# Optimization experiments

Hardware: AMD Instinct MI355X
Metric: run time of the kernel (lower is better)

The kernel has to match this reference:

```python
import jax, jax.numpy as jnp
import numpy as np

N_HEAD = 16
LORA_DIM = 16
LORA_ALPHA = 32


def setup_inputs() -> dict:
    key = jax.random.key(0)
    ks = jax.random.split(key, 8)
    B, S, D = 2, 2048, 1024
    std = 0.02
    return {
        "x": jax.random.normal(ks[0], (B, S, D), jnp.float32),
        "c_attn_w": jax.random.normal(ks[1], (D, 3 * D), jnp.float32) * std,
        "c_attn_b": jnp.zeros((3 * D,), jnp.float32),
        "c_proj_w": jax.random.normal(ks[2], (D, D), jnp.float32) * std,
        "c_proj_b": jnp.zeros((D,), jnp.float32),
        "q_a1": jax.random.normal(ks[3], (D, LORA_DIM), jnp.float32) * std,
        "q_a2": jax.random.normal(ks[4], (LORA_DIM, D), jnp.float32) * std,
        "v_a1": jax.random.normal(ks[5], (D, LORA_DIM), jnp.float32) * std,
        "v_a2": jax.random.normal(ks[6], (LORA_DIM, D), jnp.float32) * std,
    }


def reference(x, c_attn_w, c_attn_b, c_proj_w, c_proj_b, q_a1, q_a2, v_a1, v_a2):
    B, S, D = x.shape
    H = N_HEAD
    hd = D // H
    # NOTE: original code uses adapter_dim / adapter_alpha as the scale
    lora_scale = jnp.float32(LORA_DIM / LORA_ALPHA)

    qkv = x @ c_attn_w + c_attn_b                      # [B,S,3D]
    q, k, v = jnp.split(qkv, 3, axis=-1)
    q = q + ((x @ q_a1) @ q_a2) * lora_scale
    v = v + ((x @ v_a1) @ v_a2) * lora_scale

    def heads(t):
        return t.reshape(B, S, H, hd).transpose(0, 2, 1, 3)  # [B,H,S,hd]

    qh, kh, vh = heads(q), heads(k), heads(v)

    w = jnp.einsum('bhqd,bhkd->bhqk', qh, kh) / jnp.sqrt(jnp.float32(hd))
    bias = jnp.tril(jnp.ones((S, S), dtype=w.dtype))   # causal mask
    w = w * bias - jnp.float32(1e10) * (1 - bias)
    w = jax.nn.softmax(w, axis=-1)
    a = jnp.einsum('bhqk,bhkd->bhqd', w, vh)
    a = a.transpose(0, 2, 1, 3).reshape(B, S, D)       # merge heads
    a = a @ c_proj_w + c_proj_b

    present = jnp.stack((kh, vh))                      # [2,B,H,S,hd]
    return a, present
```

## Files before the change

### kernel.cpp

```cpp
#include <hip/hip_runtime.h>

#define T_TOK 4096
#define D_DIM 1024
#define N3    3072
#define S_LEN 2048
#define NH    16
#define HD    64
#define KAUG  1056

#define OUT_A_ELEMS   4194304
#define OUT_KV_ELEMS  4194304

typedef __attribute__((ext_vector_type(8))) short bf16x8;
typedef __attribute__((ext_vector_type(4))) float f32x4;
typedef __attribute__((ext_vector_type(16))) float f32x16;
typedef _Float16 f16x8 __attribute__((ext_vector_type(8)));
typedef _Float16 f16x4 __attribute__((ext_vector_type(4)));

union U4h { unsigned u[4]; f16x8 v; };

#define GHASH(r) ((((r) >> 1) ^ ((r) >> 3)) & 3)

__device__ __forceinline__ unsigned short f2bf(float f) {
    unsigned u = __float_as_uint(f);
    u += 0x7FFFu + ((u >> 16) & 1u);
    return (unsigned short)(u >> 16);
}
__device__ __forceinline__ float bf2f(unsigned short h) {
    return __uint_as_float(((unsigned)h) << 16);
}
__device__ __forceinline__ unsigned cvtpkh(float a, float b) {
    unsigned r;
    asm("v_cvt_pkrtz_f16_f32 %0, %1, %2" : "=v"(r) : "v"(a), "v"(b));
    return r;
}

#define GLL16(gp, lp) __builtin_amdgcn_global_load_lds( \
    (const __attribute__((address_space(1))) unsigned int*)(gp), \
    (__attribute__((address_space(3))) unsigned int*)(lp), 16, 0, 0)

#define MFMA16F(A, B, C) __builtin_amdgcn_mfma_f32_16x16x32_f16(A, B, C, 0, 0, 0)
#define MFMA32F(A, B, C) __builtin_amdgcn_mfma_f32_32x32x16_f16(A, B, C, 0, 0, 0)

__global__ __launch_bounds__(256) void lora1_v2(const float* __restrict__ x,
    const float* __restrict__ qa1, const float* __restrict__ va1,
    float* __restrict__ tq, float* __restrict__ tv) {
    int tid = threadIdx.x;
    int w = tid >> 6;
    int lane = tid & 63;
    int t = blockIdx.x * 4 + w;
    int cg = lane & 7;
    int ks = lane >> 3;
    const float* a1 = (cg < 4) ? qa1 : va1;
    int c4 = (cg & 3) * 4;
    const float* xr = x + (size_t)t * D_DIM + ks * 128;
    const float* ar = a1 + (size_t)(ks * 128) * 16 + c4;
    float4 acc = make_float4(0.f, 0.f, 0.f, 0.f);
#pragma unroll 8
    for (int j = 0; j < 128; ++j) {
        float xv = xr[j];
        float4 av = *(const float4*)&ar[j * 16];
        acc.x = fmaf(xv, av.x, acc.x);
        acc.y = fmaf(xv, av.y, acc.y);
        acc.z = fmaf(xv, av.z, acc.z);
        acc.w = fmaf(xv, av.w, acc.w);
    }
#pragma unroll
    for (int m = 8; m < 64; m <<= 1) {
        acc.x += __shfl_xor(acc.x, m);
        acc.y += __shfl_xor(acc.y, m);
        acc.z += __shfl_xor(acc.z, m);
        acc.w += __shfl_xor(acc.w, m);
    }
    if (lane < 8) {
        float* dst = (cg < 4) ? &tq[t * 16 + c4] : &tv[t * 16 + (cg - 4) * 4];
        *(float4*)dst = acc;
    }
}

__global__ __launch_bounds__(256) void splitA_f16(const float* __restrict__ x,
    const float* __restrict__ tq, const float* __restrict__ tv,
    _Float16* __restrict__ af) {
    int idx = blockIdx.x * 256 + threadIdx.x;
    const int total = T_TOK * (KAUG / 4);
    if (idx >= total) return;
    int t = idx / (KAUG / 4);
    int c4 = (idx - t * (KAUG / 4)) * 4;
    float4 v;
    if (c4 < D_DIM)           v = *(const float4*)&x[(size_t)t * D_DIM + c4];
    else if (c4 < D_DIM + 16) v = *(const float4*)&tq[t * 16 + (c4 - D_DIM)];
    else                      v = *(const float4*)&tv[t * 16 + (c4 - D_DIM - 16)];
    f16x4 h;
    h[0] = (_Float16)v.x; h[1] = (_Float16)v.y;
    h[2] = (_Float16)v.z; h[3] = (_Float16)v.w;
    *(f16x4*)&af[(size_t)t * KAUG + c4] = h;
}

__global__ __launch_bounds__(256) void splitW_f16(const float* __restrict__ w,
    const float* __restrict__ qa2, const float* __restrict__ va2,
    _Float16* __restrict__ bf) {
    __shared__ float T[32][65];
    int bn = blockIdx.x;
    int bk = blockIdx.y;
    int tid = threadIdx.x;
#pragma unroll
    for (int u = 0; u < 2; ++u) {
        int id = tid + 256 * u;
        int kr = id >> 4;
        int n4 = (id & 15) * 4;
        int k = bk * 32 + kr;
        int n = bn * 64 + n4;
        float4 v = make_float4(0.f, 0.f, 0.f, 0.f);
        if (k < D_DIM) {
            v = *(const float4*)&w[(size_t)k * N3 + n];
        } else if (k < D_DIM + 16) {
            if (n < D_DIM) {
                float4 q4 = *(const float4*)&qa2[(k - D_DIM) * D_DIM + n];
                v = make_float4(q4.x * 0.5f, q4.y * 0.5f, q4.z * 0.5f, q4.w * 0.5f);
            }
        } else {
            if (n >= 2 * D_DIM) {
                float4 q4 = *(const float4*)&va2[(k - D_DIM - 16) * D_DIM + (n - 2 * D_DIM)];
                v = make_float4(q4.x * 0.5f, q4.y * 0.5f, q4.z * 0.5f, q4.w * 0.5f);
            }
        }
        T[kr][n4 + 0] = v.x; T[kr][n4 + 1] = v.y;
        T[kr][n4 + 2] = v.z; T[kr][n4 + 3] = v.w;
    }
    __syncthreads();
    int n = tid >> 2;
    int k8 = (tid & 3) * 8;
    f16x8 hv;
#pragma unroll
    for (int j = 0; j < 8; ++j) hv[j] = (_Float16)T[k8 + j][n];
    int nr = bn * 64 + n;
    int gsw = (tid & 3) ^ GHASH(nr);
    size_t ro = (size_t)nr * KAUG + bk * 32 + gsw * 8;
    *(f16x8*)&bf[ro] = hv;
}

__global__ __launch_bounds__(256) void wprep_f16(const float* __restrict__ w,
    _Float16* __restrict__ bf) {
    __shared__ float T[32][65];
    int bn = blockIdx.x;
    int bk = blockIdx.y;
    int tid = threadIdx.x;
#pragma unroll
    for (int u = 0; u < 2; ++u) {
        int id = tid + 256 * u;
        int kr = id >> 4;
        int n4 = (id & 15) * 4;
        float4 v = *(const float4*)&w[(size_t)(bk * 32 + kr) * D_DIM + bn * 64 + n4];
        T[kr][n4 + 0] = v.x; T[kr][n4 + 1] = v.y;
        T[kr][n4 + 2] = v.z; T[kr][n4 + 3] = v.w;
    }
    __syncthreads();
    int n = tid >> 2;
    int k8 = (tid & 3) * 8;
    f16x8 hv;
#pragma unroll
    for (int j = 0; j < 8; ++j) hv[j] = (_Float16)T[k8 + j][n];
    int nr = bn * 64 + n;
    int gsw = (tid & 3) ^ GHASH(nr);
    size_t ro = (size_t)nr * D_DIM + bk * 32 + gsw * 8;
    *(f16x8*)&bf[ro] = hv;
}

__global__ __launch_bounds__(256, 3) void qkv_mfma(
    const _Float16* __restrict__ a_g, const _Float16* __restrict__ b_g,
    const float* __restrict__ bias,
    float* __restrict__ qstage, float* __restrict__ pres) {
    __shared__ _Float16 Bf[2][128 * 32];
    int id = blockIdx.y * 24 + blockIdx.x;
    int nid = (id & 7) * 96 + (id >> 3);
    int bn = nid % 24;
    int bm = nid / 24;
    int tid = threadIdx.x;
    int w = tid >> 6, l = tid & 63;
    int wr = w >> 1, wc = w & 1;

    f32x4 acc[4][4];
#pragma unroll
    for (int i = 0; i < 4; ++i)
#pragma unroll
        for (int j = 0; j < 4; ++j)
            acc[i][j] = (f32x4){0.f, 0.f, 0.f, 0.f};

    int srow = l >> 2;
    int sk = (l & 3) * 8;
    const size_t b_base0 = (size_t)(bn * 128 + w * 32 + srow) * KAUG + sk;
    const size_t b_base1 = b_base0 + (size_t)16 * KAUG;
    const int ldso0 = (w * 32) * 32;
    const int ldso1 = (w * 32 + 16) * 32;

    int lrow = l & 15;
    int lg = l >> 4;

    const _Float16* aF[4];
#pragma unroll
    for (int i = 0; i < 4; ++i) {
        int row = bm * 128 + wr * 64 + i * 16 + lrow;
        aF[i] = a_g + (size_t)row * KAUG + lg * 8;
    }
    int roB[4];
#pragma unroll
    for (int j = 0; j < 4; ++j) {
        int Rb = wc * 64 + j * 16 + lrow;
        roB[j] = Rb * 32 + ((lg ^ GHASH(Rb)) * 8);
    }

    f16x8 cA[4], nA[4];

    GLL16(b_g + b_base0, &Bf[0][ldso0]);
    GLL16(b_g + b_base1, &Bf[0][ldso1]);
#pragma unroll
    for (int i = 0; i < 4; ++i) cA[i] = *(const f16x8*)(aF[i]);
    asm volatile("s_waitcnt vmcnt(0)" ::: "memory");
    __builtin_amdgcn_s_barrier();

    const int NT = KAUG / 32;
    for (int t = 0; t < NT; ++t) {
        int cur = t & 1;
        if (t + 1 < NT) {
            int kn = (t + 1) * 32;
            GLL16(b_g + b_base0 + kn, &Bf[cur ^ 1][ldso0]);
            GLL16(b_g + b_base1 + kn, &Bf[cur ^ 1][ldso1]);
            __builtin_amdgcn_sched_barrier(0);
#pragma unroll
            for (int i = 0; i < 4; ++i) nA[i] = *(const f16x8*)(aF[i] + kn);
        }
        f16x8 fb[4];
#pragma unroll
        for (int j = 0; j < 4; ++j) fb[j] = *(const f16x8*)&Bf[cur][roB[j]];
#pragma unroll
        for (int i = 0; i < 4; ++i)
#pragma unroll
            for (int j = 0; j < 4; ++j)
                acc[i][j] = MFMA16F(cA[i], fb[j], acc[i][j]);
        if (t + 1 < NT) {
            asm volatile("s_waitcnt vmcnt(4)" ::: "memory");
            __builtin_amdgcn_s_barrier();
#pragma unroll
            for (int i = 0; i < 4; ++i) cA[i] = nA[i];
        }
    }

    int seg = bn >> 3;
#pragma unroll
    for (int j = 0; j < 4; ++j) {
        int n = bn * 128 + wc * 64 + j * 16 + lrow;
        float bz = bias[n];
        int h = (n >> 6) & 15;
        int d = n & 63;
#pragma unroll
        for (int i = 0; i < 4; ++i) {
            int tbase = bm * 128 + wr * 64 + i * 16 + (l >> 4) * 4;
#pragma unroll
            for (int r = 0; r < 4; ++r) {
                int t = tbase + r;
                float v = acc[i][j][r] + bz;
                int bb = t >> 11, s = t & 2047;
                size_t idx = (((size_t)(bb * NH + h) * S_LEN + s) * HD) + d;
                if (seg == 0)      qstage[idx] = v * 0.125f;
                else if (seg == 1) pres[idx] = v;
                else               pres[OUT_KV_ELEMS + idx] = v;
            }
        }
    }
}

__global__ __launch_bounds__(256, 3) void proj_mfma(
    const _Float16* __restrict__ a_g, const _Float16* __restrict__ b_g,
    const float* __restrict__ bias, float* __restrict__ outp) {
    __shared__ _Float16 Bf[2][128 * 32];
    int id = blockIdx.y * 8 + blockIdx.x;
    int nid = (id & 7) * 32 + (id >> 3);
    int bn = nid % 8;
    int bm = nid / 8;
    int tid = threadIdx.x;
    int w = tid >> 6, l = tid & 63;
    int wr = w >> 1, wc = w & 1;

    f32x4 acc[4][4];
#pragma unroll
    for (int i = 0; i < 4; ++i)
#pragma unroll
        for (int j = 0; j < 4; ++j)
            acc[i][j] = (f32x4){0.f, 0.f, 0.f, 0.f};

    int srow = l >> 2;
    int sk = (l & 3) * 8;
    const size_t b_base0 = (size_t)(bn * 128 + w * 32 + srow) * D_DIM + sk;
    const size_t b_base1 = b_base0 + (size_t)16 * D_DIM;
    const int ldso0 = (w * 32) * 32;
    const int ldso1 = (w * 32 + 16) * 32;

    int lrow = l & 15;
    int lg = l >> 4;

    const _Float16* aF[4];
#pragma unroll
    for (int i = 0; i < 4; ++i) {
        int row = bm * 128 + wr * 64 + i * 16 + lrow;
        aF[i] = a_g + (size_t)row * D_DIM + lg * 8;
    }
    int roB[4];
#pragma unroll
    for (int j = 0; j < 4; ++j) {
        int Rb = wc * 64 + j * 16 + lrow;
        roB[j] = Rb * 32 + ((lg ^ GHASH(Rb)) * 8);
    }

    f16x8 cA[4], nA[4];

    GLL16(b_g + b_base0, &Bf[0][ldso0]);
    GLL16(b_g + b_base1, &Bf[0][ldso1]);
#pragma unroll
    for (int i = 0; i < 4; ++i) cA[i] = *(const f16x8*)(aF[i]);
    asm volatile("s_waitcnt vmcnt(0)" ::: "memory");
    __builtin_amdgcn_s_barrier();

    const int NT = D_DIM / 32;
    for (int t = 0; t < NT; ++t) {
        int cur = t & 1;
        if (t + 1 < NT) {
            int kn = (t + 1) * 32;
            GLL16(b_g + b_base0 + kn, &Bf[cur ^ 1][ldso0]);
            GLL16(b_g + b_base1 + kn, &Bf[cur ^ 1][ldso1]);
            __builtin_amdgcn_sched_barrier(0);
#pragma unroll
            for (int i = 0; i < 4; ++i) nA[i] = *(const f16x8*)(aF[i] + kn);
        }
        f16x8 fb[4];
#pragma unroll
        for (int j = 0; j < 4; ++j) fb[j] = *(const f16x8*)&Bf[cur][roB[j]];
#pragma unroll
        for (int i = 0; i < 4; ++i)
#pragma unroll
            for (int j = 0; j < 4; ++j)
                acc[i][j] = MFMA16F(cA[i], fb[j], acc[i][j]);
        if (t + 1 < NT) {
            asm volatile("s_waitcnt vmcnt(4)" ::: "memory");
            __builtin_amdgcn_s_barrier();
#pragma unroll
            for (int i = 0; i < 4; ++i) cA[i] = nA[i];
        }
    }

#pragma unroll
    for (int j = 0; j < 4; ++j) {
        int n = bn * 128 + wc * 64 + j * 16 + lrow;
        float bz = bias[n];
#pragma unroll
        for (int i = 0; i < 4; ++i) {
            int tbase = bm * 128 + wr * 64 + i * 16 + (l >> 4) * 4;
#pragma unroll
            for (int r = 0; r < 4; ++r)
                outp[(size_t)(tbase + r) * D_DIM + n] = acc[i][j][r] + bz;
        }
    }
}

__global__ __launch_bounds__(256) void kprep_f16(const float* __restrict__ kin,
    _Float16* __restrict__ kp) {
    int id = blockIdx.x * 256 + threadIdx.x;
    int rowi = id >> 3;
    int gsrc = id & 7;
    const float* src = kin + (size_t)rowi * 64 + gsrc * 8;
    float4 v0 = *(const float4*)src;
    float4 v1 = *(const float4*)(src + 4);
    int key = rowi & 2047;
    int gp = gsrc ^ (key & 7);
    float vv[8] = {v0.x, v0.y, v0.z, v0.w, v1.x, v1.y, v1.z, v1.w};
    f16x8 h;
#pragma unroll
    for (int j = 0; j < 8; ++j) h[j] = (_Float16)vv[j];
    *(f16x8*)&kp[(size_t)rowi * 64 + gp * 8] = h;
}

__global__ __launch_bounds__(256) void vtprep_f16(const float* __restrict__ vin,
    _Float16* __restrict__ vt) {
    __shared__ __align__(16) _Float16 T[64][72];
    int bh = blockIdx.x;
    int kv0 = blockIdx.y * 64;
    int tid = threadIdx.x;
#pragma unroll
    for (int p = 0; p < 4; ++p) {
        int key = (tid >> 4) + 16 * p;
        int d0 = (tid & 15) * 4;
        float4 v = *(const float4*)&vin[((size_t)bh * 2048 + kv0 + key) * 64 + d0];
        T[d0 + 0][key] = (_Float16)v.x;
        T[d0 + 1][key] = (_Float16)v.y;
        T[d0 + 2][key] = (_Float16)v.z;
        T[d0 + 3][key] = (_Float16)v.w;
    }
    __syncthreads();
    int d = tid >> 2;
#pragma unroll
    for (int q = 0; q < 2; ++q) {
        int gg = (tid & 3) + 4 * q;
        int gs = gg ^ (d & 7);
        f16x8 hv = *(const f16x8*)&T[d][gs * 8];
        size_t dst = ((size_t)bh * 64 + d) * 2048 + kv0 + gg * 8;
        *(f16x8*)&vt[dst] = hv;
    }
}

__device__ __forceinline__ void stage_tile(
    const _Float16* __restrict__ kp, const _Float16* __restrict__ vt,
    _Float16 (*ldsb)[4096], int w, int l, int bh, int kv0) {
    if (w < 2) {
        const _Float16* gp = kp
            + ((size_t)bh * 2048 + kv0 + w * 32 + (l >> 3)) * 64 + (l & 7) * 8;
        _Float16* lp = ldsb[0] + (w * 32) * 64;
#pragma unroll
        for (int i = 0; i < 4; ++i)
            GLL16(gp + i * 512, lp + i * 512);
    } else {
        int wv = w - 2;
        const _Float16* gp = vt
            + ((size_t)bh * 64 + wv * 32 + (l >> 3)) * 2048 + kv0 + (l & 7) * 8;
        _Float16* lp = ldsb[1] + (wv * 32) * 64;
#pragma unroll
        for (int i = 0; i < 4; ++i)
            GLL16(gp + (size_t)i * 8 * 2048, lp + i * 512);
    }
}

#define QROW(r) ((((r) & 3) + 8 * ((r) >> 2)) + 4 * g)

__global__ __launch_bounds__(256, 4) void attn_mfma(
    const float* __restrict__ q_s,
    const _Float16* __restrict__ kp, const _Float16* __restrict__ vt,
    _Float16* __restrict__ aout) {
    __shared__ __align__(16) _Float16 lds[2][2][4096];
    int bh = blockIdx.x;
    int qi = (int)gridDim.y - 1 - blockIdx.y;
    int tid = threadIdx.x;
    int w = tid >> 6, l = tid & 63;
    int qloc = l & 31, g = l >> 5;
    int q0 = qi * 128;
    int qg = q0 + w * 32 + qloc;

    f16x8 qf[4];
    {
        const float* qrow = q_s + ((size_t)bh * S_LEN + qg) * HD;
#pragma unroll
        for (int t = 0; t < 4; ++t) {
            f16x8 r;
#pragma unroll
            for (int j = 0; j < 8; ++j)
                r[j] = (_Float16)qrow[t * 16 + g * 8 + j];
            qf[t] = r;
        }
    }

    f32x16 o0, o1;
#pragma unroll
    for (int r = 0; r < 16; ++r) { o0[r] = 0.f; o1[r] = 0.f; }
    float m_run = -1e30f, l_run = 0.f;

    int nt = 2 * qi + 2;
    int qwmax = q0 + w * 32 + 31;

    stage_tile(kp, vt, lds[0], w, l, bh, 0);
    __syncthreads();

    for (int t = 0; t < nt; ++t) {
        int kv0 = t * 64;
        int bi = t & 1;
        if (t + 1 < nt)
            stage_tile(kp, vt, lds[bi ^ 1], w, l, bh, (t + 1) * 64);

        if (kv0 <= qwmax) {
            const _Float16* Kp = lds[bi][0];
            const _Float16* Vp = lds[bi][1];

            f32x16 s0, s1;
#pragma unroll
            for (int r = 0; r < 16; ++r) { s0[r] = 0.f; s1[r] = 0.f; }

            __builtin_amdgcn_s_setprio(1);
#pragma unroll
            for (int tt = 0; tt < 4; ++tt) {
                int gr = ((2 * tt + g) ^ (qloc & 7)) * 8;
                f16x8 a0 = *(const f16x8*)&Kp[qloc * 64 + gr];
                f16x8 a1 = *(const f16x8*)&Kp[(32 + qloc) * 64 + gr];
                s0 = MFMA32F(a0, qf[tt], s0);
                s1 = MFMA32F(a1, qf[tt], s1);
            }
            __builtin_amdgcn_s_setprio(0);

            if (kv0 + 63 > q0 + w * 32) {
#pragma unroll
                for (int r = 0; r < 16; ++r) {
                    int kk = kv0 + QROW(r);
                    if (kk > qg)      s0[r] = -1e30f;
                    if (kk + 32 > qg) s1[r] = -1e30f;
                }
            }

            float mx = s0[0];
#pragma unroll
            for (int r = 1; r < 16; ++r) mx = fmaxf(mx, s0[r]);
#pragma unroll
            for (int r = 0; r < 16; ++r) mx = fmaxf(mx, s1[r]);
            mx = fmaxf(mx, __shfl_xor(mx, 32));
            float mnew = fmaxf(m_run, mx);
            float al = __expf(m_run - mnew);
            m_run = mnew;
            float rs = 0.f;
#pragma unroll
            for (int r = 0; r < 16; ++r) { s0[r] = __expf(s0[r] - mnew); rs += s0[r]; }
#pragma unroll
            for (int r = 0; r < 16; ++r) { s1[r] = __expf(s1[r] - mnew); rs += s1[r]; }
            rs += __shfl_xor(rs, 32);
            l_run = l_run * al + rs;
#pragma unroll
            for (int r = 0; r < 16; ++r) {
                float ar = __shfl(al, QROW(r));
                o0[r] *= ar; o1[r] *= ar;
            }

            __builtin_amdgcn_s_setprio(1);
#pragma unroll
            for (int ks = 0; ks < 4; ++ks) {
                const int b = (ks & 1) * 8;
                unsigned w0, w1, w2, w3;
                if (ks < 2) {
                    w0 = cvtpkh(s0[b + 0], s0[b + 1]);
                    w1 = cvtpkh(s0[b + 2], s0[b + 3]);
                    w2 = cvtpkh(s0[b + 4], s0[b + 5]);
                    w3 = cvtpkh(s0[b + 6], s0[b + 7]);
                } else {
                    w0 = cvtpkh(s1[b + 0], s1[b + 1]);
                    w1 = cvtpkh(s1[b + 2], s1[b + 3]);
                    w2 = cvtpkh(s1[b + 4], s1[b + 5]);
                    w3 = cvtpkh(s1[b + 6], s1[b + 7]);
                }
                asm("v_permlane32_swap_b32 %0, %1" : "+v"(w0), "+v"(w2));
                asm("v_permlane32_swap_b32 %0, %1" : "+v"(w1), "+v"(w3));
                U4h u; u.u[0] = w0; u.u[1] = w1; u.u[2] = w2; u.u[3] = w3;
                f16x8 pa = u.v;
                int gr = ((2 * ks + g) ^ (qloc & 7)) * 8;
                f16x8 v0 = *(const f16x8*)&Vp[qloc * 64 + gr];
                f16x8 v1 = *(const f16x8*)&Vp[(32 + qloc) * 64 + gr];
                o0 = MFMA32F(pa, v0, o0);
                o1 = MFMA32F(pa, v1, o1);
            }
            __builtin_amdgcn_s_setprio(0);
        }
        __syncthreads();
    }

    int bb = bh >> 4, h = bh & 15;
#pragma unroll
    for (int r = 0; r < 16; ++r) {
        float li = __shfl(l_run, QROW(r));
        float inv = 1.f / li;
        int qq = q0 + w * 32 + QROW(r);
        size_t base = ((size_t)(bb * S_LEN + qq)) * D_DIM + h * HD + qloc;
        aout[base]      = (_Float16)(o0[r] * inv);
        aout[base + 32] = (_Float16)(o1[r] * inv);
    }
}

#define LSTR 68
__global__ __launch_bounds__(256) void attn_kernel(const float* __restrict__ q_s,
    const float* __restrict__ k_s, const float* __restrict__ v_s,
    float* __restrict__ a_s) {
    __shared__ float Qt[64][LSTR];
    __shared__ float KP[64][LSTR];
    __shared__ float Vs[64][LSTR];
    int bh = blockIdx.x;
    int qi = 31 - blockIdx.y;
    int tid = threadIdx.x;
    int tx = tid & 15, ty = tid >> 4;

#pragma unroll
    for (int qq = 0; qq < 4; ++qq) {
        int q  = qq * 16 + (tid >> 4);
        int d4 = (tid & 15) * 4;
        float4 v = *(const float4*)&q_s[((size_t)bh * S_LEN + qi * 64 + q) * HD + d4];
        Qt[d4 + 0][q] = v.x; Qt[d4 + 1][q] = v.y;
        Qt[d4 + 2][q] = v.z; Qt[d4 + 3][q] = v.w;
    }

    float o[4][4];
#pragma unroll
    for (int r = 0; r < 4; ++r)
#pragma unroll
        for (int c = 0; c < 4; ++c) o[r][c] = 0.f;
    float mrow[4] = {-1e30f, -1e30f, -1e30f, -1e30f};
    float lrow[4] = {0.f, 0.f, 0.f, 0.f};

    for (int kt = 0; kt <= qi; ++kt) {
        __syncthreads();
#pragma unroll
        for (int kk2 = 0; kk2 < 4; ++kk2) {
            int k  = kk2 * 16 + (tid >> 4);
            int d4 = (tid & 15) * 4;
            size_t rowoff = ((size_t)bh * S_LEN + kt * 64 + k) * HD + d4;
            float4 kv4 = *(const float4*)&k_s[rowoff];
            KP[d4 + 0][k] = kv4.x; KP[d4 + 1][k] = kv4.y;
            KP[d4 + 2][k] = kv4.z; KP[d4 + 3][k] = kv4.w;
            float4 vv4 = *(const float4*)&v_s[rowoff];
            *(float4*)&Vs[k][d4] = vv4;
        }
        __syncthreads();

        float s[4][4];
#pragma unroll
        for (int r = 0; r < 4; ++r)
#pragma unroll
            for (int c = 0; c < 4; ++c) s[r][c] = 0.f;
#pragma unroll 8
        for (int d = 0; d < 64; ++d) {
            float4 qv = *(const float4*)&Qt[d][ty * 4];
            float4 kv = *(const float4*)&KP[d][tx * 4];
            float qa[4] = {qv.x, qv.y, qv.z, qv.w};
            float ka[4] = {kv.x, kv.y, kv.z, kv.w};
#pragma unroll
            for (int r = 0; r < 4; ++r)
#pragma unroll
                for (int c = 0; c < 4; ++c)
                    s[r][c] = fmaf(qa[r], ka[c], s[r][c]);
        }
        if (kt == qi) {
#pragma unroll
            for (int r = 0; r < 4; ++r)
#pragma unroll
                for (int c = 0; c < 4; ++c)
                    if (tx * 4 + c > ty * 4 + r) s[r][c] = -1e30f;
        }
        __syncthreads();

        float p[4][4];
#pragma unroll
        for (int r = 0; r < 4; ++r) {
            float mx = fmaxf(fmaxf(s[r][0], s[r][1]), fmaxf(s[r][2], s[r][3]));
            mx = fmaxf(mx, __shfl_xor(mx, 1));
            mx = fmaxf(mx, __shfl_xor(mx, 2));
            mx = fmaxf(mx, __shfl_xor(mx, 4));
            mx = fmaxf(mx, __shfl_xor(mx, 8));
            float mn = fmaxf(mrow[r], mx);
            float alpha = __expf(mrow[r] - mn);
            mrow[r] = mn;
            float rsum = 0.f;
#pragma unroll
            for (int c = 0; c < 4; ++c) {
                p[r][c] = __expf(s[r][c] - mn);
                rsum += p[r][c];
            }
            rsum += __shfl_xor(rsum, 1);
            rsum += __shfl_xor(rsum, 2);
            rsum += __shfl_xor(rsum, 4);
            rsum += __shfl_xor(rsum, 8);
            lrow[r] = lrow[r] * alpha + rsum;
#pragma unroll
            for (int c = 0; c < 4; ++c) o[r][c] *= alpha;
            *(float4*)&KP[ty * 4 + r][tx * 4] =
                make_float4(p[r][0], p[r][1], p[r][2], p[r][3]);
        }
        __syncthreads();

#pragma unroll 8
        for (int k = 0; k < 64; ++k) {
            float4 vv = *(const float4*)&Vs[k][tx * 4];
            float va[4] = {vv.x, vv.y, vv.z, vv.w};
#pragma unroll
            for (int r = 0; r < 4; ++r) {
                float pr = KP[ty * 4 + r][k];
#pragma unroll
                for (int c = 0; c < 4; ++c)
                    o[r][c] = fmaf(pr, va[c], o[r][c]);
            }
        }
    }

    int b = bh >> 4, h = bh & 15;
#pragma unroll
    for (int r = 0; r < 4; ++r) {
        int i = qi * 64 + ty * 4 + r;
        float inv = 1.f / lrow[r];
        *(float4*)&a_s[((size_t)(b * S_LEN + i)) * D_DIM + h * HD + tx * 4] =
            make_float4(o[r][0] * inv, o[r][1] * inv, o[r][2] * inv, o[r][3] * inv);
    }
}

__global__ __launch_bounds__(256) void proj_kernel(const float* __restrict__ A,
    const float* __restrict__ w, const float* __restrict__ bias,
    float* __restrict__ outp) {
    __shared__ float As[128][17];
    __shared__ float Bs[16][64];
    int bx = blockIdx.x;
    int by = blockIdx.y;
    int tid = threadIdx.x;
    int tx = tid & 15, ty = tid >> 4;

    float c[8][4];
#pragma unroll
    for (int i = 0; i < 8; ++i)
#pragma unroll
        for (int j = 0; j < 4; ++j) c[i][j] = 0.f;

    for (int k0 = 0; k0 < D_DIM; k0 += 16) {
#pragma unroll
        for (int u = 0; u < 2; ++u) {
            int f4 = tid + 256 * u;
            int row = f4 >> 2;
            int kk4 = (f4 & 3) * 4;
            float4 av = *(const float4*)&A[(size_t)(by * 128 + row) * D_DIM + k0 + kk4];
            As[row][kk4 + 0] = av.x; As[row][kk4 + 1] = av.y;
            As[row][kk4 + 2] = av.z; As[row][kk4 + 3] = av.w;
        }
        {
            int kkb = tid >> 4;
            int col4 = (tid & 15) * 4;
            *(float4*)&Bs[kkb][col4] =
                *(const float4*)&w[(size_t)(k0 + kkb) * D_DIM + bx * 64 + col4];
        }
        __syncthreads();
#pragma unroll
        for (int kk = 0; kk < 16; ++kk) {
            float4 bv = *(const float4*)&Bs[kk][tx * 4];
#pragma unroll
            for (int i = 0; i < 8; ++i) {
                float a = As[ty * 8 + i][kk];
                c[i][0] = fmaf(a, bv.x, c[i][0]);
                c[i][1] = fmaf(a, bv.y, c[i][1]);
                c[i][2] = fmaf(a, bv.z, c[i][2]);
                c[i][3] = fmaf(a, bv.w, c[i][3]);
            }
        }
        __syncthreads();
    }

    int ncol = bx * 64 + tx * 4;
    float4 bias4 = *(const float4*)&bias[ncol];
#pragma unroll
    for (int i = 0; i < 8; ++i) {
        int t = by * 128 + ty * 8 + i;
        *(float4*)&outp[(size_t)t * D_DIM + ncol] =
            make_float4(c[i][0] + bias4.x, c[i][1] + bias4.y,
                        c[i][2] + bias4.z, c[i][3] + bias4.w);
    }
}

extern "C" void kernel_launch(void* const* d_in, const int* in_sizes, int n_in,
                              void* d_out, int out_size, void* d_ws, size_t ws_size,
                              hipStream_t stream) {
    const float* x        = (const float*)d_in[0];
    const float* c_attn_w = (const float*)d_in[1];
    const float* c_attn_b = (const float*)d_in[2];
    const float* c_proj_w = (const float*)d_in[3];
    const float* c_proj_b = (const float*)d_in[4];
    const float* q_a1     = (const float*)d_in[5];
    const float* q_a2     = (const float*)d_in[6];
    const float* v_a1     = (const float*)d_in[7];
    const float* v_a2     = (const float*)d_in[8];

    float* outf   = (float*)d_out;
    float* qstage = outf;
    float* pres   = outf + OUT_A_ELEMS;

    char* wsb = (char*)d_ws;
    float* tq = (float*)wsb;
    float* tv = (float*)(wsb + 262144);
    _Float16* w_f16  = (_Float16*)(wsb + 524288);
    _Float16* a_f16  = (_Float16*)(wsb + 7012352);
    _Float16* kp_f16 = (_Float16*)(wsb + 16777216);
    _Float16* vt_f16 = (_Float16*)(wsb + 25165824);
    _Float16* aout_f16 = (_Float16*)wsb;
    _Float16* wp_f16   = (_Float16*)(wsb + 8388608);
    const size_t WS_FULL = 33554432;
    const size_t WS_MID  = 16777216;

    lora1_v2<<<dim3(1024), dim3(256), 0, stream>>>(x, q_a1, v_a1, tq, tv);

    if (ws_size >= WS_FULL) {
        splitA_f16<<<dim3((T_TOK * (KAUG / 4) + 255) / 256), dim3(256), 0, stream>>>(
            x, tq, tv, a_f16);
        splitW_f16<<<dim3(48, KAUG / 32), dim3(256), 0, stream>>>(
            c_attn_w, q_a2, v_a2, w_f16);
        qkv_mfma<<<dim3(24, 32), dim3(256), 0, stream>>>(
            a_f16, w_f16, c_attn_b, qstage, pres);
        kprep_f16<<<dim3(2048), dim3(256), 0, stream>>>(pres, kp_f16);
        vtprep_f16<<<dim3(32, 32), dim3(256), 0, stream>>>(
            pres + OUT_KV_ELEMS, vt_f16);
        attn_mfma<<<dim3(32, 16), dim3(256), 0, stream>>>(
            qstage, kp_f16, vt_f16, aout_f16);
        wprep_f16<<<dim3(16, 32), dim3(256), 0, stream>>>(c_proj_w, wp_f16);
        proj_mfma<<<dim3(8, 32), dim3(256), 0, stream>>>(
            aout_f16, wp_f16, c_proj_b, outf);
    } else if (ws_size >= WS_MID) {
        float* a_s = (float*)wsb;
        splitA_f16<<<dim3((T_TOK * (KAUG / 4) + 255) / 256), dim3(256), 0, stream>>>(
            x, tq, tv, a_f16);
        splitW_f16<<<dim3(48, KAUG / 32), dim3(256), 0, stream>>>(
            c_attn_w, q_a2, v_a2, w_f16);
        qkv_mfma<<<dim3(24, 32), dim3(256), 0, stream>>>(
            a_f16, w_f16, c_attn_b, qstage, pres);
        attn_kernel<<<dim3(32, 32), dim3(256), 0, stream>>>(
            qstage, pres, pres + OUT_KV_ELEMS, a_s);
        proj_kernel<<<dim3(16, 32), dim3(256), 0, stream>>>(
            a_s, c_proj_w, c_proj_b, outf);
    } else {
        float* a_s2 = tv + 65536;
        attn_kernel<<<dim3(32, 32), dim3(256), 0, stream>>>(
            qstage, pres, pres + OUT_KV_ELEMS, a_s2);
        proj_kernel<<<dim3(16, 32), dim3(256), 0, stream>>>(
            a_s2, c_proj_w, c_proj_b, outf);
    }
}
```

Before: 260.5 us.

## Fuse K/V f16 prep into QKV GEMM epilogue and double K-step per barrier

The QKV GEMM epilogue now writes the swizzled f16 K copy, the transposed f16 V copy and an f16 Q buffer directly, so the separate kprep/vtprep kernels and the f32 Q reload-and-convert in attention go away. Both GEMMs now process two 32-wide K slices per loop iteration with doubled LDS buffers, which halves the barrier count. The cost is more scattered stores in the epilogue, more LDS per block that may lower occupancy, and a larger workspace requirement for the full path.

Result: faster. 250.8 us (-3.8%).

```diff
diff --git a/kernel.cpp b/kernel.cpp
--- a/kernel.cpp
+++ b/kernel.cpp
@@ -11,7 +11,6 @@
 #define OUT_A_ELEMS   4194304
 #define OUT_KV_ELEMS  4194304
 
-typedef __attribute__((ext_vector_type(8))) short bf16x8;
 typedef __attribute__((ext_vector_type(4))) float f32x4;
 typedef __attribute__((ext_vector_type(16))) float f32x16;
 typedef _Float16 f16x8 __attribute__((ext_vector_type(8)));
@@ -21,14 +20,6 @@
 
 #define GHASH(r) ((((r) >> 1) ^ ((r) >> 3)) & 3)
 
-__device__ __forceinline__ unsigned short f2bf(float f) {
-    unsigned u = __float_as_uint(f);
-    u += 0x7FFFu + ((u >> 16) & 1u);
-    return (unsigned short)(u >> 16);
-}
-__device__ __forceinline__ float bf2f(unsigned short h) {
-    return __uint_as_float(((unsigned)h) << 16);
-}
 __device__ __forceinline__ unsigned cvtpkh(float a, float b) {
     unsigned r;
     asm("v_cvt_pkrtz_f16_f32 %0, %1, %2" : "=v"(r) : "v"(a), "v"(b));
@@ -168,9 +159,11 @@
 
 __global__ __launch_bounds__(256, 3) void qkv_mfma(
     const _Float16* __restrict__ a_g, const _Float16* __restrict__ b_g,
-    const float* __restrict__ bias,
-    float* __restrict__ qstage, float* __restrict__ pres) {
-    __shared__ _Float16 Bf[2][128 * 32];
+    const float* __restrict__ bias, int mode,
+    float* __restrict__ qstage, float* __restrict__ pres,
+    _Float16* __restrict__ qf16, _Float16* __restrict__ kp,
+    _Float16* __restrict__ vt) {
+    __shared__ _Float16 Bf[2][2][128 * 32];
     int id = blockIdx.y * 24 + blockIdx.x;
     int nid = (id & 7) * 96 + (id >> 3);
     int bn = nid % 24;
@@ -209,61 +202,115 @@
         roB[j] = Rb * 32 + ((lg ^ GHASH(Rb)) * 8);
     }
 
-    f16x8 cA[4], nA[4];
-
-    GLL16(b_g + b_base0, &Bf[0][ldso0]);
-    GLL16(b_g + b_base1, &Bf[0][ldso1]);
-#pragma unroll
-    for (int i = 0; i < 4; ++i) cA[i] = *(const f16x8*)(aF[i]);
+    f16x8 cA0[4], cA1[4], nA0[4], nA1[4];
+
+    GLL16(b_g + b_base0,      &Bf[0][0][ldso0]);
+    GLL16(b_g + b_base1,      &Bf[0][0][ldso1]);
+    GLL16(b_g + b_base0 + 32, &Bf[0][1][ldso0]);
+    GLL16(b_g + b_base1 + 32, &Bf[0][1][ldso1]);
+#pragma unroll
+    for (int i = 0; i < 4; ++i) {
+        cA0[i] = *(const f16x8*)(aF[i]);
+        cA1[i] = *(const f16x8*)(aF[i] + 32);
+    }
     asm volatile("s_waitcnt vmcnt(0)" ::: "memory");
     __builtin_amdgcn_s_barrier();
 
-    const int NT = KAUG / 32;
-    for (int t = 0; t < NT; ++t) {
-        int cur = t & 1;
-        if (t + 1 < NT) {
-            int kn = (t + 1) * 32;
-            GLL16(b_g + b_base0 + kn, &Bf[cur ^ 1][ldso0]);
-            GLL16(b_g + b_base1 + kn, &Bf[cur ^ 1][ldso1]);
+    for (int r = 0; r < 17; ++r) {
+        int cur = r & 1;
+        if (r < 16) {
+            int kn = (r + 1) * 64;
+            GLL16(b_g + b_base0 + kn, &Bf[cur ^ 1][0][ldso0]);
+            GLL16(b_g + b_base1 + kn, &Bf[cur ^ 1][0][ldso1]);
+            if (r < 15) {
+                GLL16(b_g + b_base0 + kn + 32, &Bf[cur ^ 1][1][ldso0]);
+                GLL16(b_g + b_base1 + kn + 32, &Bf[cur ^ 1][1][ldso1]);
+            }
             __builtin_amdgcn_sched_barrier(0);
 #pragma unroll
-            for (int i = 0; i < 4; ++i) nA[i] = *(const f16x8*)(aF[i] + kn);
+            for (int i = 0; i < 4; ++i) nA0[i] = *(const f16x8*)(aF[i] + kn);
+            if (r < 15) {
+#pragma unroll
+                for (int i = 0; i < 4; ++i) nA1[i] = *(const f16x8*)(aF[i] + kn + 32);
+            }
         }
         f16x8 fb[4];
 #pragma unroll
-        for (int j = 0; j < 4; ++j) fb[j] = *(const f16x8*)&Bf[cur][roB[j]];
+        for (int j = 0; j < 4; ++j) fb[j] = *(const f16x8*)&Bf[cur][0][roB[j]];
 #pragma unroll
         for (int i = 0; i < 4; ++i)
 #pragma unroll
             for (int j = 0; j < 4; ++j)
-                acc[i][j] = MFMA16F(cA[i], fb[j], acc[i][j]);
-        if (t + 1 < NT) {
-            asm volatile("s_waitcnt vmcnt(4)" ::: "memory");
+                acc[i][j] = MFMA16F(cA0[i], fb[j], acc[i][j]);
+        if (r < 16) {
+#pragma unroll
+            for (int j = 0; j < 4; ++j) fb[j] = *(const f16x8*)&Bf[cur][1][roB[j]];
+#pragma unroll
+            for (int i = 0; i < 4; ++i)
+#pragma unroll
+                for (int j = 0; j < 4; ++j)
+                    acc[i][j] = MFMA16F(cA1[i], fb[j], acc[i][j]);
+            if (r < 15) asm volatile("s_waitcnt vmcnt(8)" ::: "memory");
+            else        asm volatile("s_waitcnt vmcnt(4)" ::: "memory");
             __builtin_amdgcn_s_barrier();
 #pragma unroll
-            for (int i = 0; i < 4; ++i) cA[i] = nA[i];
+            for (int i = 0; i < 4; ++i) cA0[i] = nA0[i];
+            if (r < 15) {
+#pragma unroll
+                for (int i = 0; i < 4; ++i) cA1[i] = nA1[i];
+            }
         }
     }
 
     int seg = bn >> 3;
+    int bb = bm >> 4;
 #pragma unroll
     for (int j = 0; j < 4; ++j) {
         int n = bn * 128 + wc * 64 + j * 16 + lrow;
         float bz = bias[n];
         int h = (n >> 6) & 15;
         int d = n & 63;
+        size_t rowbase = (size_t)(bb * NH + h) * S_LEN;
 #pragma unroll
         for (int i = 0; i < 4; ++i) {
-            int tbase = bm * 128 + wr * 64 + i * 16 + (l >> 4) * 4;
-#pragma unroll
-            for (int r = 0; r < 4; ++r) {
-                int t = tbase + r;
-                float v = acc[i][j][r] + bz;
-                int bb = t >> 11, s = t & 2047;
-                size_t idx = (((size_t)(bb * NH + h) * S_LEN + s) * HD) + d;
-                if (seg == 0)      qstage[idx] = v * 0.125f;
-                else if (seg == 1) pres[idx] = v;
-                else               pres[OUT_KV_ELEMS + idx] = v;
+            int tb = bm * 128 + wr * 64 + i * 16 + (l >> 4) * 4;
+            int s0 = tb & 2047;
+            if (seg == 0) {
+                if (mode == 0) {
+#pragma unroll
+                    for (int r = 0; r < 4; ++r)
+                        qf16[(rowbase + s0 + r) * HD + d] =
+                            (_Float16)((acc[i][j][r] + bz) * 0.125f);
+                } else {
+#pragma unroll
+                    for (int r = 0; r < 4; ++r)
+                        qstage[(rowbase + s0 + r) * HD + d] =
+                            (acc[i][j][r] + bz) * 0.125f;
+                }
+            } else if (seg == 1) {
+                int gsw = d >> 3;
+#pragma unroll
+                for (int r = 0; r < 4; ++r) {
+                    float v = acc[i][j][r] + bz;
+                    int s = s0 + r;
+                    pres[(rowbase + s) * HD + d] = v;
+                    if (mode == 0)
+                        kp[(rowbase + s) * HD + ((gsw ^ (s & 7)) << 3) + (d & 7)] =
+                            (_Float16)v;
+                }
+            } else {
+                f16x4 pk;
+#pragma unroll
+                for (int r = 0; r < 4; ++r) {
+                    float v = acc[i][j][r] + bz;
+                    pres[OUT_KV_ELEMS + (rowbase + s0 + r) * HD + d] = v;
+                    pk[r] = (_Float16)v;
+                }
+                if (mode == 0) {
+                    int gp = ((s0 >> 3) & 7) ^ (d & 7);
+                    *(f16x4*)&vt[((size_t)(bb * NH + h) * 64 + d) * 2048
+                                 + (s0 & ~63) + (gp << 3) + (s0 & 7)] = pk;
+                }
             }
         }
     }
@@ -272,7 +319,7 @@
 __global__ __launch_bounds__(256, 3) void proj_mfma(
     const _Float16* __restrict__ a_g, const _Float16* __restrict__ b_g,
     const float* __restrict__ bias, float* __restrict__ outp) {
-    __shared__ _Float16 Bf[2][128 * 32];
+    __shared__ _Float16 Bf[2][2][128 * 32];
     int id = blockIdx.y * 8 + blockIdx.x;
     int nid = (id & 7) * 32 + (id >> 3);
     int bn = nid % 8;
@@ -311,39 +358,55 @@
         roB[j] = Rb * 32 + ((lg ^ GHASH(Rb)) * 8);
     }
 
-    f16x8 cA[4], nA[4];
-
-    GLL16(b_g + b_base0, &Bf[0][ldso0]);
-    GLL16(b_g + b_base1, &Bf[0][ldso1]);
-#pragma unroll
-    for (int i = 0; i < 4; ++i) cA[i] = *(const f16x8*)(aF[i]);
+    f16x8 cA0[4], cA1[4], nA0[4], nA1[4];
+
+    GLL16(b_g + b_base0,      &Bf[0][0][ldso0]);
+    GLL16(b_g + b_base1,      &Bf[0][0][ldso1]);
+    GLL16(b_g + b_base0 + 32, &Bf[0][1][ldso0]);
+    GLL16(b_g + b_base1 + 32, &Bf[0][1][ldso1]);
+#pragma unroll
+    for (int i = 0; i < 4; ++i) {
+        cA0[i] = *(const f16x8*)(aF[i]);
+        cA1[i] = *(const f16x8*)(aF[i] + 32);
+    }
     asm volatile("s_waitcnt vmcnt(0)" ::: "memory");
     __builtin_amdgcn_s_barrier();
 
-    const int NT = D_DIM / 32;
-    for (int t = 0; t < NT; ++t) {
-        int cur = t & 1;
-        if (t + 1 < NT) {
-            int kn = (t + 1) * 32;
-            GLL16(b_g + b_base0 + kn, &Bf[cur ^ 1][ldso0]);
-            GLL16(b_g + b_base1 + kn, &Bf[cur ^ 1][ldso1]);
+    for (int r = 0; r < 16; ++r) {
+        int cur = r & 1;
+        if (r < 15) {
+            int kn = (r + 1) * 64;
+            GLL16(b_g + b_base0 + kn,      &Bf[cur ^ 1][0][ldso0]);
+            GLL16(b_g + b_base1 + kn,      &Bf[cur ^ 1][0][ldso1]);
+            GLL16(b_g + b_base0 + kn + 32, &Bf[cur ^ 1][1][ldso0]);
+            GLL16(b_g + b_base1 + kn + 32, &Bf[cur ^ 1][1][ldso1]);
             __builtin_amdgcn_sched_barrier(0);
 #pragma unroll
-            for (int i = 0; i < 4; ++i) nA[i] = *(const f16x8*)(aF[i] + kn);
+            for (int i = 0; i < 4; ++i) {
+                nA0[i] = *(const f16x8*)(aF[i] + kn);
+                nA1[i] = *(const f16x8*)(aF[i] + kn + 32);
+            }
         }
         f16x8 fb[4];
 #pragma unroll
-        for (int j = 0; j < 4; ++j) fb[j] = *(const f16x8*)&Bf[cur][roB[j]];
+        for (int j = 0; j < 4; ++j) fb[j] = *(const f16x8*)&Bf[cur][0][roB[j]];
 #pragma unroll
         for (int i = 0; i < 4; ++i)
 #pragma unroll
             for (int j = 0; j < 4; ++j)
-                acc[i][j] = MFMA16F(cA[i], fb[j], acc[i][j]);
-        if (t + 1 < NT) {
-            asm volatile("s_waitcnt vmcnt(4)" ::: "memory");
+                acc[i][j] = MFMA16F(cA0[i], fb[j], acc[i][j]);
+#pragma unroll
+        for (int j = 0; j < 4; ++j) fb[j] = *(const f16x8*)&Bf[cur][1][roB[j]];
+#pragma unroll
+        for (int i = 0; i < 4; ++i)
+#pragma unroll
+            for (int j = 0; j < 4; ++j)
+                acc[i][j] = MFMA16F(cA1[i], fb[j], acc[i][j]);
+        if (r < 15) {
+            asm volatile("s_waitcnt vmcnt(8)" ::: "memory");
             __builtin_amdgcn_s_barrier();
 #pragma unroll
-            for (int i = 0; i < 4; ++i) cA[i] = nA[i];
+            for (int i = 0; i < 4; ++i) { cA0[i] = nA0[i]; cA1[i] = nA1[i]; }
         }
     }
 
@@ -358,51 +421,6 @@
             for (int r = 0; r < 4; ++r)
                 outp[(size_t)(tbase + r) * D_DIM + n] = acc[i][j][r] + bz;
         }
-    }
-}
-
-__global__ __launch_bounds__(256) void kprep_f16(const float* __restrict__ kin,
-    _Float16* __restrict__ kp) {
-    int id = blockIdx.x * 256 + threadIdx.x;
-    int rowi = id >> 3;
-    int gsrc = id & 7;
-    const float* src = kin + (size_t)rowi * 64 + gsrc * 8;
-    float4 v0 = *(const float4*)src;
-    float4 v1 = *(const float4*)(src + 4);
-    int key = rowi & 2047;
-    int gp = gsrc ^ (key & 7);
-    float vv[8] = {v0.x, v0.y, v0.z, v0.w, v1.x, v1.y, v1.z, v1.w};
-    f16x8 h;
-#pragma unroll
-    for (int j = 0; j < 8; ++j) h[j] = (_Float16)vv[j];
-    *(f16x8*)&kp[(size_t)rowi * 64 + gp * 8] = h;
-}
-
-__global__ __launch_bounds__(256) void vtprep_f16(const float* __restrict__ vin,
-    _Float16* __restrict__ vt) {
-    __shared__ __align__(16) _Float16 T[64][72];
-    int bh = blockIdx.x;
-    int kv0 = blockIdx.y * 64;
-    int tid = threadIdx.x;
-#pragma unroll
-    for (int p = 0; p < 4; ++p) {
-        int key = (tid >> 4) + 16 * p;
-        int d0 = (tid & 15) * 4;
-        float4 v = *(const float4*)&vin[((size_t)bh * 2048 + kv0 + key) * 64 + d0];
-        T[d0 + 0][key] = (_Float16)v.x;
-        T[d0 + 1][key] = (_Float16)v.y;
-        T[d0 + 2][key] = (_Float16)v.z;
-        T[d0 + 3][key] = (_Float16)v.w;
-    }
-    __syncthreads();
-    int d = tid >> 2;
-#pragma unroll
-    for (int q = 0; q < 2; ++q) {
-        int gg = (tid & 3) + 4 * q;
-        int gs = gg ^ (d & 7);
-        f16x8 hv = *(const f16x8*)&T[d][gs * 8];
-        size_t dst = ((size_t)bh * 64 + d) * 2048 + kv0 + gg * 8;
-        *(f16x8*)&vt[dst] = hv;
     }
 }
 
@@ -430,7 +448,7 @@
 #define QROW(r) ((((r) & 3) + 8 * ((r) >> 2)) + 4 * g)
 
 __global__ __launch_bounds__(256, 4) void attn_mfma(
-    const float* __restrict__ q_s,
+    const _Float16* __restrict__ q_h,
     const _Float16* __restrict__ kp, const _Float16* __restrict__ vt,
     _Float16* __restrict__ aout) {
     __shared__ __align__(16) _Float16 lds[2][2][4096];
@@ -444,15 +462,10 @@
 
     f16x8 qf[4];
     {
-        const float* qrow = q_s + ((size_t)bh * S_LEN + qg) * HD;
-#pragma unroll
-        for (int t = 0; t < 4; ++t) {
-            f16x8 r;
-#pragma unroll
-            for (int j = 0; j < 8; ++j)
-                r[j] = (_Float16)qrow[t * 16 + g * 8 + j];
-            qf[t] = r;
-        }
+        const _Float16* qrow = q_h + ((size_t)bh * S_LEN + qg) * HD;
+#pragma unroll
+        for (int t = 0; t < 4; ++t)
+            qf[t] = *(const f16x8*)&qrow[t * 16 + g * 8];
     }
 
     f32x16 o0, o1;
@@ -771,9 +784,10 @@
     _Float16* a_f16  = (_Float16*)(wsb + 7012352);
     _Float16* kp_f16 = (_Float16*)(wsb + 16777216);
     _Float16* vt_f16 = (_Float16*)(wsb + 25165824);
+    _Float16* q_h16  = (_Float16*)(wsb + 33554432);
     _Float16* aout_f16 = (_Float16*)wsb;
     _Float16* wp_f16   = (_Float16*)(wsb + 8388608);
-    const size_t WS_FULL = 33554432;
+    const size_t WS_FULL = 41943040;
     const size_t WS_MID  = 16777216;
 
     lora1_v2<<<dim3(1024), dim3(256), 0, stream>>>(x, q_a1, v_a1, tq, tv);
@@ -784,12 +798,9 @@
         splitW_f16<<<dim3(48, KAUG / 32), dim3(256), 0, stream>>>(
             c_attn_w, q_a2, v_a2, w_f16);
         qkv_mfma<<<dim3(24, 32), dim3(256), 0, stream>>>(
-            a_f16, w_f16, c_attn_b, qstage, pres);
-        kprep_f16<<<dim3(2048), dim3(256), 0, stream>>>(pres, kp_f16);
-        vtprep_f16<<<dim3(32, 32), dim3(256), 0, stream>>>(
-            pres + OUT_KV_ELEMS, vt_f16);
+            a_f16, w_f16, c_attn_b, 0, nullptr, pres, q_h16, kp_f16, vt_f16);
         attn_mfma<<<dim3(32, 16), dim3(256), 0, stream>>>(
-            qstage, kp_f16, vt_f16, aout_f16);
+            q_h16, kp_f16, vt_f16, aout_f16);
         wprep_f16<<<dim3(16, 32), dim3(256), 0, stream>>>(c_proj_w, wp_f16);
         proj_mfma<<<dim3(8, 32), dim3(256), 0, stream>>>(
             aout_f16, wp_f16, c_proj_b, outf);
@@ -800,7 +811,7 @@
         splitW_f16<<<dim3(48, KAUG / 32), dim3(256), 0, stream>>>(
             c_attn_w, q_a2, v_a2, w_f16);
         qkv_mfma<<<dim3(24, 32), dim3(256), 0, stream>>>(
-            a_f16, w_f16, c_attn_b, qstage, pres);
+            a_f16, w_f16, c_attn_b, 1, qstage, pres, nullptr, nullptr, nullptr);
         attn_kernel<<<dim3(32, 32), dim3(256), 0, stream>>>(
             qstage, pres, pres + OUT_KV_ELEMS, a_s);
         proj_kernel<<<dim3(16, 32), dim3(256), 0, stream>>>(
```
